# Kernel optimization log

Hardware: AMD Instinct MI355X
Metric: run time of the kernel (lower is better)

Reference implementation:

```python
import jax, jax.numpy as jnp
import numpy as np

B, T, D, H = 2, 4096, 768, 12
DH = D // H


def setup_inputs() -> dict:
    key = jax.random.key(0)
    ks = jax.random.split(key, 4)
    x = jax.random.normal(ks[0], (B, T, D), dtype=jnp.float32)
    Wqkv = jax.random.normal(ks[1], (D, 3 * D), dtype=jnp.float32) * (D ** -0.5)
    bqkv = jnp.zeros((3 * D,), dtype=jnp.float32)
    Wproj = jax.random.normal(ks[2], (D, D), dtype=jnp.float32) * (D ** -0.5)
    bproj = jnp.zeros((D,), dtype=jnp.float32)
    return {"x": x, "Wqkv": Wqkv, "bqkv": bqkv, "Wproj": Wproj, "bproj": bproj}


def reference(x, Wqkv, bqkv, Wproj, bproj):
    b, t, c = x.shape
    qkv = x @ Wqkv + bqkv                      # [B,T,3D]
    qkv = qkv.reshape(b, t, H, 3 * DH)
    q, k, v = jnp.split(qkv, 3, axis=-1)       # each [B,T,H,DH]
    q = q.transpose(0, 2, 1, 3)                # [B,H,T,DH]
    k = k.transpose(0, 2, 1, 3)
    v = v.transpose(0, 2, 1, 3)
    att = jnp.einsum('bhqd,bhkd->bhqk', q, k) / (DH ** 0.5)  # [B,H,T,T]
    mask = jnp.tril(jnp.ones((t, t), dtype=bool))
    att = jnp.where(mask, att, jnp.float32(-1e9))
    att = jax.nn.softmax(att, axis=-1)
    out = jnp.einsum('bhqk,bhkd->bhqd', att, v)  # [B,H,T,DH]
    out = out.transpose(0, 2, 1, 3).reshape(b, t, c)
    return out @ Wproj + bproj
```

## Files before the change

kernel.cpp:

```cpp
#include <hip/hip_runtime.h>

typedef unsigned short u16;
typedef unsigned int u32;
typedef __bf16 bf16x8 __attribute__((ext_vector_type(8)));
typedef float f32x4 __attribute__((ext_vector_type(4)));
typedef float f32x16 __attribute__((ext_vector_type(16)));
typedef u16 u16x4 __attribute__((ext_vector_type(4)));
typedef u16 u16x8 __attribute__((ext_vector_type(8)));
typedef u32 u32x2 __attribute__((ext_vector_type(2)));
typedef u32 u32x4 __attribute__((ext_vector_type(4)));

#define QSCALE 0.18033688011112042f
#define MFIX 12.0f

static __device__ __forceinline__ u16 f2bf(float f) {
  __bf16 h = (__bf16)f;
  return __builtin_bit_cast(u16, h);
}

static __device__ __forceinline__ u32 pk2(float a, float b) {
  return (u32)f2bf(a) | ((u32)f2bf(b) << 16);
}

static __device__ __forceinline__ void gl_lds16(const void* g, void* l) {
  __builtin_amdgcn_global_load_lds(
      (const __attribute__((address_space(1))) unsigned int*)g,
      (__attribute__((address_space(3))) unsigned int*)l, 16, 0, 0);
}

static __device__ __forceinline__ void wait_vmcnt8() {
  asm volatile("s_waitcnt vmcnt(8)" ::: "memory");
}
static __device__ __forceinline__ void wait_vmcnt4() {
  asm volatile("s_waitcnt vmcnt(4)" ::: "memory");
}
static __device__ __forceinline__ void wait_vmcnt0() {
  asm volatile("s_waitcnt vmcnt(0)" ::: "memory");
}
static __device__ __forceinline__ void barrier_mem() {
  asm volatile("s_barrier" ::: "memory");
}

static __device__ __forceinline__ f32x16 zero16() {
  f32x16 z;
#pragma unroll
  for (int i = 0; i < 16; ++i) z[i] = 0.f;
  return z;
}

__global__ void k_cvt(const float* __restrict__ in, u16* __restrict__ out, int n4) {
  int i = blockIdx.x * 256 + threadIdx.x;
  if (i < n4) {
    f32x4 f = ((const f32x4*)in)[i];
    u16x4 u = { f2bf(f[0]), f2bf(f[1]), f2bf(f[2]), f2bf(f[3]) };
    ((u16x4*)out)[i] = u;
  }
}

__global__ void k_transpose_cvt(const float* __restrict__ in, u16* __restrict__ out,
                                int R, int C) {
  __shared__ float tile[32][33];
  const int c0 = blockIdx.x * 32, r0 = blockIdx.y * 32;
  const int tx = threadIdx.x, ty = threadIdx.y;
#pragma unroll
  for (int i = 0; i < 4; ++i)
    tile[ty + i * 8][tx] = in[(size_t)(r0 + ty + i * 8) * C + c0 + tx];
  __syncthreads();
#pragma unroll
  for (int i = 0; i < 4; ++i)
    out[(size_t)(c0 + ty + i * 8) * R + r0 + tx] = f2bf(tile[tx][ty + i * 8]);
}

static __device__ __forceinline__ void gemm_core(const u16* __restrict__ Ag,
                                                 const u16* __restrict__ Btg,
                                                 int K, int m0, int n0,
                                                 u16* As, u16* Bs,
                                                 f32x4 acc[4][4]) {
  const int tid = threadIdx.x;
  const int lane = tid & 63;
  const int wid = tid >> 6;
  const int wm = wid >> 1, wn = wid & 1;
  const int l16 = lane & 15, lg = lane >> 4;

  for (int kt = 0; kt < K; kt += 64) {
    __syncthreads();
#pragma unroll
    for (int i = 0; i < 4; ++i) {
      int chunk = i * 256 + tid;
      int row = chunk >> 3;
      int lcb = ((chunk & 7) << 4) ^ ((row & 7) << 4);
      gl_lds16(Ag + (size_t)(m0 + row) * K + kt + (lcb >> 1),
               As + ((i * 256 + wid * 64) << 3));
    }
#pragma unroll
    for (int i = 0; i < 4; ++i) {
      int chunk = i * 256 + tid;
      int row = chunk >> 3;
      int lcb = ((chunk & 7) << 4) ^ ((row & 7) << 4);
      gl_lds16(Btg + (size_t)(n0 + row) * K + kt + (lcb >> 1),
               Bs + ((i * 256 + wid * 64) << 3));
    }
    __syncthreads();

#pragma unroll
    for (int ks = 0; ks < 2; ++ks) {
      bf16x8 af[4], bfr[4];
#pragma unroll
      for (int mi = 0; mi < 4; ++mi) {
        int row = wm * 64 + mi * 16 + l16;
        int off = row * 128 + ((ks * 64 + (lg << 4)) ^ ((row & 7) << 4));
        af[mi] = *(const bf16x8*)((const char*)As + off);
      }
#pragma unroll
      for (int ni = 0; ni < 4; ++ni) {
        int row = wn * 64 + ni * 16 + l16;
        int off = row * 128 + ((ks * 64 + (lg << 4)) ^ ((row & 7) << 4));
        bfr[ni] = *(const bf16x8*)((const char*)Bs + off);
      }
#pragma unroll
      for (int mi = 0; mi < 4; ++mi)
#pragma unroll
        for (int ni = 0; ni < 4; ++ni)
          acc[mi][ni] = __builtin_amdgcn_mfma_f32_16x16x32_bf16(
              af[mi], bfr[ni], acc[mi][ni], 0, 0, 0);
    }
  }
}

__global__ __launch_bounds__(256) void k_gemm_qkv(
    const u16* __restrict__ A, const u16* __restrict__ Bt,
    const float* __restrict__ bias, u16* __restrict__ Q, u16* __restrict__ Kb,
    u16* __restrict__ Vt) {
  __shared__ __align__(16) u16 SH[128 * 128];
  u16* As = SH;
  u16* Bs = SH + 128 * 64;
  const int m0 = blockIdx.y * 128, n0 = blockIdx.x * 128;
  const f32x4 fz = {0.f, 0.f, 0.f, 0.f};
  f32x4 acc[4][4];
#pragma unroll
  for (int mi = 0; mi < 4; ++mi)
#pragma unroll
    for (int ni = 0; ni < 4; ++ni) acc[mi][ni] = fz;

  gemm_core(A, Bt, 768, m0, n0, As, Bs, acc);
  __syncthreads();

  const int tid = threadIdx.x, lane = tid & 63, wid = tid >> 6;
  const int wm = wid >> 1, wn = wid & 1, l16 = lane & 15, lg = lane >> 4;
#pragma unroll
  for (int mi = 0; mi < 4; ++mi)
#pragma unroll
    for (int ni = 0; ni < 4; ++ni) {
      int nl = wn * 64 + ni * 16 + l16;
      int n = n0 + nl;
      float bi = bias[n];
      int h = n / 192;
      int rr = n - h * 192;
      int ml = wm * 64 + mi * 16 + lg * 4;
      if (rr >= 128) {
        int m0w = m0 + ml;
        int bb = m0w >> 12, t0 = m0w & 4095;
        u16x4 vv;
#pragma unroll
        for (int r = 0; r < 4; ++r) vv[r] = f2bf(acc[mi][ni][r] + bi);
        *(u16x4*)(Vt + ((size_t)(bb * 12 + h) * 64 + (rr - 128)) * 4096 + t0) = vv;
      } else {
        float sc = (rr < 64) ? QSCALE : 1.0f;
#pragma unroll
        for (int r = 0; r < 4; ++r)
          SH[(ml + r) * 128 + nl] = f2bf((acc[mi][ni][r] + bi) * sc);
      }
    }
  __syncthreads();

  const int bb2 = m0 >> 12, tb = m0 & 4095;
#pragma unroll
  for (int i = 0; i < 8; ++i) {
    int id = i * 256 + tid;
    int row = id >> 4;
    int c = id & 15;
    int n = n0 + c * 8;
    int h = n / 192;
    int rr = n - h * 192;
    if (rr < 128) {
      u16x8 v = *(const u16x8*)(SH + row * 128 + c * 8);
      size_t base = ((size_t)(bb2 * 12 + h) * 4096 + tb + row) * 64;
      u16* dst = (rr < 64) ? (Q + base + rr) : (Kb + base + rr - 64);
      *(u16x8*)dst = v;
    }
  }
}

__global__ __launch_bounds__(256) void k_gemm_proj(
    const u16* __restrict__ A, const u16* __restrict__ Bt,
    const float* __restrict__ bias, float* __restrict__ out) {
  __shared__ __align__(16) u16 As[128 * 64];
  __shared__ __align__(16) u16 Bs[128 * 64];
  const int m0 = blockIdx.y * 128, n0 = blockIdx.x * 128;
  const f32x4 fz = {0.f, 0.f, 0.f, 0.f};
  f32x4 acc[4][4];
#pragma unroll
  for (int mi = 0; mi < 4; ++mi)
#pragma unroll
    for (int ni = 0; ni < 4; ++ni) acc[mi][ni] = fz;

  gemm_core(A, Bt, 768, m0, n0, As, Bs, acc);

  const int tid = threadIdx.x, lane = tid & 63, wid = tid >> 6;
  const int wm = wid >> 1, wn = wid & 1, l16 = lane & 15, lg = lane >> 4;
#pragma unroll
  for (int mi = 0; mi < 4; ++mi)
#pragma unroll
    for (int ni = 0; ni < 4; ++ni) {
      int n = n0 + wn * 64 + ni * 16 + l16;
      float bi = bias[n];
#pragma unroll
      for (int r = 0; r < 4; ++r) {
        int m = m0 + wm * 64 + mi * 16 + lg * 4 + r;
        out[(size_t)m * 768 + n] = acc[mi][ni][r] + bi;
      }
    }
}

__global__ __launch_bounds__(128) void k_attn(const u16* __restrict__ Qg,
                                              const u16* __restrict__ Kg,
                                              const u16* __restrict__ Vtg,
                                              u16* __restrict__ Og) {
  __shared__ __align__(16) u16 Ks[2][64 * 64];
  __shared__ __align__(16) u16 Vs[64 * 64];
  const int bid = blockIdx.x;
  const int xcd = bid & 7;
  const int u = bid >> 3;
  const int s = u & 31;
  const int rnd = u >> 5;
  const int bh = xcd * 3 + (rnd >> 1);
  const int jX = (rnd & 1) ? s : (63 - s);
  const int tid = threadIdx.x;
  const int lane = tid & 63;
  const int wid = tid >> 6;
  const int l32 = lane & 31;
  const int hi = lane >> 5;
  const int rxor = (l32 & 7) << 4;
  const size_t qk_base = (size_t)bh * (4096 * 64);
  const size_t vt_base = (size_t)bh * (64 * 4096);
  const int b = bh / 12, h = bh - b * 12;

  const int q0w = jX * 64 + wid * 32;
  const int qrow = q0w + l32;
  const int nkt = jX + 1;

  int coK[4], coVa[4], coVb[4];
#pragma unroll
  for (int st = 0; st < 4; ++st) coK[st] = (st * 32 + hi * 16) ^ rxor;
#pragma unroll
  for (int ks = 0; ks < 4; ++ks) {
    coVa[ks] = (ks * 32 + hi * 8) ^ rxor;
    coVb[ks] = (ks * 32 + 16 + hi * 8) ^ rxor;
  }
  const int rb0 = l32 * 128, rb1 = (32 + l32) * 128;

  const int trow = tid >> 3;
  const int tcol = ((((tid & 7) << 4) ^ ((trow & 7) << 4)) >> 1);
  const int tdst = tid << 3;
  const u16* kp0 = Kg + qk_base + (size_t)trow * 64 + tcol;
  const u16* kp1 = kp0 + (size_t)16 * 64;
  const u16* kp2 = kp0 + (size_t)32 * 64;
  const u16* kp3 = kp0 + (size_t)48 * 64;
  const u16* vq0 = Vtg + vt_base + (size_t)trow * 4096 + tcol;
  const u16* vq1 = vq0 + (size_t)16 * 4096;
  const u16* vq2 = vq0 + (size_t)32 * 4096;
  const u16* vq3 = vq0 + (size_t)48 * 4096;

  auto stageK = [&](u16* Kd) {
    gl_lds16(kp0, Kd + tdst);
    gl_lds16(kp1, Kd + 1024 + tdst);
    gl_lds16(kp2, Kd + 2048 + tdst);
    gl_lds16(kp3, Kd + 3072 + tdst);
    kp0 += 4096; kp1 += 4096; kp2 += 4096; kp3 += 4096;
  };
  auto stageV = [&]() {
    gl_lds16(vq0, Vs + tdst);
    gl_lds16(vq1, Vs + 1024 + tdst);
    gl_lds16(vq2, Vs + 2048 + tdst);
    gl_lds16(vq3, Vs + 3072 + tdst);
    vq0 += 64; vq1 += 64; vq2 += 64; vq3 += 64;
  };

  bf16x8 qb[4];
#pragma unroll
  for (int st = 0; st < 4; ++st)
    qb[st] = *(const bf16x8*)(Qg + qk_base + (size_t)qrow * 64 + st * 16 + hi * 8);

  f32x16 o0 = zero16(), o1 = zero16();
  float lrun = 0.f;

  stageK(Ks[0]);

  for (int kt = 0; kt < nkt; ++kt) {
    const bool more = (kt + 1 < nkt);
    stageV();
    if (more) stageK(Ks[(kt + 1) & 1]);
    if (more) wait_vmcnt8(); else wait_vmcnt4();
    barrier_mem();

    const bool diag = (kt == nkt - 1);
    const bool halfskip = diag && (wid == 0);
    const char* Kbp = (const char*)Ks[kt & 1];
    const char* Vb = (const char*)Vs;

    f32x16 s0 = zero16(), s1 = zero16();
    __builtin_amdgcn_s_setprio(1);
#pragma unroll
    for (int st = 0; st < 4; ++st) {
      bf16x8 ka0 = *(const bf16x8*)(Kbp + rb0 + coK[st]);
      s0 = __builtin_amdgcn_mfma_f32_32x32x16_bf16(ka0, qb[st], s0, 0, 0, 0);
    }
    if (!halfskip) {
#pragma unroll
      for (int st = 0; st < 4; ++st) {
        bf16x8 ka1 = *(const bf16x8*)(Kbp + rb1 + coK[st]);
        s1 = __builtin_amdgcn_mfma_f32_32x32x16_bf16(ka1, qb[st], s1, 0, 0, 0);
      }
    }
    __builtin_amdgcn_s_setprio(0);

    if (diag) {
      const int kbase = kt * 64 + 4 * hi;
#pragma unroll
      for (int r = 0; r < 16; ++r) {
        int kpv = kbase + (r & 3) + 8 * (r >> 2);
        s0[r] = (kpv > qrow) ? -3.0e38f : s0[r];
        if (!halfskip) s1[r] = (kpv + 32 > qrow) ? -3.0e38f : s1[r];
      }
    }

#pragma unroll
    for (int r = 0; r < 16; ++r) {
      s0[r] = __builtin_amdgcn_exp2f(s0[r] - MFIX);
      if (!halfskip) s1[r] = __builtin_amdgcn_exp2f(s1[r] - MFIX);
    }

    float a8[8];
#pragma unroll
    for (int r = 0; r < 8; ++r) {
      float v = s0[r] + s0[r + 8];
      if (!halfskip) v += s1[r] + s1[r + 8];
      a8[r] = v;
    }
    lrun += ((a8[0] + a8[1]) + (a8[2] + a8[3])) +
            ((a8[4] + a8[5]) + (a8[6] + a8[7]));

    if (more) wait_vmcnt4(); else wait_vmcnt0();
    barrier_mem();

    __builtin_amdgcn_s_setprio(1);
#pragma unroll
    for (int ks = 0; ks < 4; ++ks) {
      if (ks >= 2 && halfskip) continue;
      const f32x16& P = (ks >= 2) ? s1 : s0;
      const int base = (ks & 1) * 8;
      u32x4 w = { pk2(P[base + 0], P[base + 1]), pk2(P[base + 2], P[base + 3]),
                  pk2(P[base + 4], P[base + 5]), pk2(P[base + 6], P[base + 7]) };
      bf16x8 pbk = __builtin_bit_cast(bf16x8, w);
      u32x2 q0 = *(const u32x2*)(Vb + rb0 + coVa[ks]);
      u32x2 q1 = *(const u32x2*)(Vb + rb0 + coVb[ks]);
      u32x4 av = {q0[0], q0[1], q1[0], q1[1]};
      bf16x8 va0 = __builtin_bit_cast(bf16x8, av);
      o0 = __builtin_amdgcn_mfma_f32_32x32x16_bf16(va0, pbk, o0, 0, 0, 0);
      u32x2 p0 = *(const u32x2*)(Vb + rb1 + coVa[ks]);
      u32x2 p1 = *(const u32x2*)(Vb + rb1 + coVb[ks]);
      u32x4 bv = {p0[0], p0[1], p1[0], p1[1]};
      bf16x8 va1 = __builtin_bit_cast(bf16x8, bv);
      o1 = __builtin_amdgcn_mfma_f32_32x32x16_bf16(va1, pbk, o1, 0, 0, 0);
    }
    __builtin_amdgcn_s_setprio(0);

    barrier_mem();
  }

  float lt = lrun + __shfl_xor(lrun, 32, 64);
  float inv = 1.0f / lt;
  u16* orow = Og + ((size_t)b * 4096 + qrow) * 768 + h * 64;
#pragma unroll
  for (int gg = 0; gg < 4; ++gg) {
    u16x4 v0, v1;
#pragma unroll
    for (int i = 0; i < 4; ++i) {
      v0[i] = f2bf(o0[4 * gg + i] * inv);
      v1[i] = f2bf(o1[4 * gg + i] * inv);
    }
    *(u16x4*)(orow + 8 * gg + 4 * hi) = v0;
    *(u16x4*)(orow + 32 + 8 * gg + 4 * hi) = v1;
  }
}

extern "C" void kernel_launch(void* const* d_in, const int* in_sizes, int n_in,
                              void* d_out, int out_size, void* d_ws, size_t ws_size,
                              hipStream_t stream) {
  const float* x = (const float*)d_in[0];
  const float* Wqkv = (const float*)d_in[1];
  const float* bqkv = (const float*)d_in[2];
  const float* Wproj = (const float*)d_in[3];
  const float* bproj = (const float*)d_in[4];
  float* out = (float*)d_out;

  char* ws = (char*)d_ws;
  u16* Xbf = (u16*)(ws + 0);
  u16* WqkvT = (u16*)(ws + 12582912);
  u16* WprojT = (u16*)(ws + 16121856);
  u16* Q = (u16*)(ws + 17301504);
  u16* K = (u16*)(ws + 29884416);
  u16* Vt = (u16*)(ws + 42467328);
  u16* O = (u16*)(ws + 55050240);

  k_cvt<<<6144, 256, 0, stream>>>(x, Xbf, 1572864);
  k_transpose_cvt<<<dim3(72, 24), dim3(32, 8), 0, stream>>>(Wqkv, WqkvT, 768, 2304);
  k_transpose_cvt<<<dim3(24, 24), dim3(32, 8), 0, stream>>>(Wproj, WprojT, 768, 768);
  k_gemm_qkv<<<dim3(18, 64), 256, 0, stream>>>(Xbf, WqkvT, bqkv, Q, K, Vt);
  k_attn<<<1536, 128, 0, stream>>>(Q, K, Vt, O);
  k_gemm_proj<<<dim3(6, 64), 256, 0, stream>>>(O, WprojT, bproj, out);
}
```

Before: 197.7 us.

## Split attention key tile across four waves with LDS reduction of partial outputs

The attention block grows from two to four waves. Each pair of waves shares a 32-row query slice and splits the 64-key tile in half, so every wave does half the QK and PV MFMAs per tile. Partial outputs and row sums are combined through LDS at the end. This doubles the waves available to hide latency and halves the staging loads per thread, at the cost of an extra reduction pass, more LDS traffic and a possible occupancy change from the new launch bounds.

```diff
diff --git a/kernel.cpp b/kernel.cpp
--- a/kernel.cpp
+++ b/kernel.cpp
@@ -28,11 +28,11 @@
       (__attribute__((address_space(3))) unsigned int*)l, 16, 0, 0);
 }
 
-static __device__ __forceinline__ void wait_vmcnt8() {
-  asm volatile("s_waitcnt vmcnt(8)" ::: "memory");
-}
 static __device__ __forceinline__ void wait_vmcnt4() {
   asm volatile("s_waitcnt vmcnt(4)" ::: "memory");
+}
+static __device__ __forceinline__ void wait_vmcnt2() {
+  asm volatile("s_waitcnt vmcnt(2)" ::: "memory");
 }
 static __device__ __forceinline__ void wait_vmcnt0() {
   asm volatile("s_waitcnt vmcnt(0)" ::: "memory");
@@ -222,12 +222,14 @@
     }
 }
 
-__global__ __launch_bounds__(128) void k_attn(const u16* __restrict__ Qg,
-                                              const u16* __restrict__ Kg,
-                                              const u16* __restrict__ Vtg,
-                                              u16* __restrict__ Og) {
-  __shared__ __align__(16) u16 Ks[2][64 * 64];
-  __shared__ __align__(16) u16 Vs[64 * 64];
+__global__ __launch_bounds__(256, 6) void k_attn(const u16* __restrict__ Qg,
+                                                 const u16* __restrict__ Kg,
+                                                 const u16* __restrict__ Vtg,
+                                                 u16* __restrict__ Og) {
+  __shared__ __align__(16) u16 LDSB[12288];
+  u16* const KsA = LDSB;
+  u16* const KsB = LDSB + 4096;
+  u16* const Vs = LDSB + 8192;
   const int bid = blockIdx.x;
   const int xcd = bid & 7;
   const int u = bid >> 3;
@@ -238,6 +240,7 @@
   const int tid = threadIdx.x;
   const int lane = tid & 63;
   const int wid = tid >> 6;
+  const int qhalf = wid >> 1, khalf = wid & 1;
   const int l32 = lane & 31;
   const int hi = lane >> 5;
   const int rxor = (l32 & 7) << 4;
@@ -245,45 +248,39 @@
   const size_t vt_base = (size_t)bh * (64 * 4096);
   const int b = bh / 12, h = bh - b * 12;
 
-  const int q0w = jX * 64 + wid * 32;
-  const int qrow = q0w + l32;
+  const int qrow = jX * 64 + qhalf * 32 + l32;
   const int nkt = jX + 1;
 
-  int coK[4], coVa[4], coVb[4];
+  int coK[4];
 #pragma unroll
   for (int st = 0; st < 4; ++st) coK[st] = (st * 32 + hi * 16) ^ rxor;
-#pragma unroll
-  for (int ks = 0; ks < 4; ++ks) {
-    coVa[ks] = (ks * 32 + hi * 8) ^ rxor;
-    coVb[ks] = (ks * 32 + 16 + hi * 8) ^ rxor;
-  }
+  int cvA[2], cvB[2];
+#pragma unroll
+  for (int kl = 0; kl < 2; ++kl) {
+    int ks = 2 * khalf + kl;
+    cvA[kl] = (ks * 32 + hi * 8) ^ rxor;
+    cvB[kl] = (ks * 32 + 16 + hi * 8) ^ rxor;
+  }
+  const int rbK = (khalf * 32 + l32) * 128;
   const int rb0 = l32 * 128, rb1 = (32 + l32) * 128;
 
   const int trow = tid >> 3;
   const int tcol = ((((tid & 7) << 4) ^ ((trow & 7) << 4)) >> 1);
   const int tdst = tid << 3;
   const u16* kp0 = Kg + qk_base + (size_t)trow * 64 + tcol;
-  const u16* kp1 = kp0 + (size_t)16 * 64;
-  const u16* kp2 = kp0 + (size_t)32 * 64;
-  const u16* kp3 = kp0 + (size_t)48 * 64;
+  const u16* kp1 = kp0 + (size_t)32 * 64;
   const u16* vq0 = Vtg + vt_base + (size_t)trow * 4096 + tcol;
-  const u16* vq1 = vq0 + (size_t)16 * 4096;
-  const u16* vq2 = vq0 + (size_t)32 * 4096;
-  const u16* vq3 = vq0 + (size_t)48 * 4096;
+  const u16* vq1 = vq0 + (size_t)32 * 4096;
 
   auto stageK = [&](u16* Kd) {
     gl_lds16(kp0, Kd + tdst);
-    gl_lds16(kp1, Kd + 1024 + tdst);
-    gl_lds16(kp2, Kd + 2048 + tdst);
-    gl_lds16(kp3, Kd + 3072 + tdst);
-    kp0 += 4096; kp1 += 4096; kp2 += 4096; kp3 += 4096;
+    gl_lds16(kp1, Kd + 2048 + tdst);
+    kp0 += 4096; kp1 += 4096;
   };
   auto stageV = [&]() {
     gl_lds16(vq0, Vs + tdst);
-    gl_lds16(vq1, Vs + 1024 + tdst);
-    gl_lds16(vq2, Vs + 2048 + tdst);
-    gl_lds16(vq3, Vs + 3072 + tdst);
-    vq0 += 64; vq1 += 64; vq2 += 64; vq3 += 64;
+    gl_lds16(vq1, Vs + 2048 + tdst);
+    vq0 += 64; vq1 += 64;
   };
 
   bf16x8 qb[4];
@@ -294,103 +291,112 @@
   f32x16 o0 = zero16(), o1 = zero16();
   float lrun = 0.f;
 
-  stageK(Ks[0]);
+  stageK(KsA);
 
   for (int kt = 0; kt < nkt; ++kt) {
     const bool more = (kt + 1 < nkt);
     stageV();
-    if (more) stageK(Ks[(kt + 1) & 1]);
-    if (more) wait_vmcnt8(); else wait_vmcnt4();
+    if (more) stageK((kt & 1) ? KsA : KsB);
+    if (more) wait_vmcnt4(); else wait_vmcnt2();
     barrier_mem();
 
     const bool diag = (kt == nkt - 1);
-    const bool halfskip = diag && (wid == 0);
-    const char* Kbp = (const char*)Ks[kt & 1];
+    const bool skip = diag && (qhalf == 0) && (khalf == 1);
+    const bool tri = diag && (qhalf == khalf);
+    const char* Kbp = (const char*)((kt & 1) ? KsB : KsA);
     const char* Vb = (const char*)Vs;
 
-    f32x16 s0 = zero16(), s1 = zero16();
-    __builtin_amdgcn_s_setprio(1);
-#pragma unroll
-    for (int st = 0; st < 4; ++st) {
-      bf16x8 ka0 = *(const bf16x8*)(Kbp + rb0 + coK[st]);
-      s0 = __builtin_amdgcn_mfma_f32_32x32x16_bf16(ka0, qb[st], s0, 0, 0, 0);
-    }
-    if (!halfskip) {
+    f32x16 s0 = zero16();
+    if (!skip) {
+      __builtin_amdgcn_s_setprio(1);
 #pragma unroll
       for (int st = 0; st < 4; ++st) {
-        bf16x8 ka1 = *(const bf16x8*)(Kbp + rb1 + coK[st]);
-        s1 = __builtin_amdgcn_mfma_f32_32x32x16_bf16(ka1, qb[st], s1, 0, 0, 0);
-      }
-    }
-    __builtin_amdgcn_s_setprio(0);
-
-    if (diag) {
-      const int kbase = kt * 64 + 4 * hi;
-#pragma unroll
-      for (int r = 0; r < 16; ++r) {
-        int kpv = kbase + (r & 3) + 8 * (r >> 2);
-        s0[r] = (kpv > qrow) ? -3.0e38f : s0[r];
-        if (!halfskip) s1[r] = (kpv + 32 > qrow) ? -3.0e38f : s1[r];
-      }
-    }
-
-#pragma unroll
-    for (int r = 0; r < 16; ++r) {
-      s0[r] = __builtin_amdgcn_exp2f(s0[r] - MFIX);
-      if (!halfskip) s1[r] = __builtin_amdgcn_exp2f(s1[r] - MFIX);
-    }
-
-    float a8[8];
-#pragma unroll
-    for (int r = 0; r < 8; ++r) {
-      float v = s0[r] + s0[r + 8];
-      if (!halfskip) v += s1[r] + s1[r + 8];
-      a8[r] = v;
-    }
-    lrun += ((a8[0] + a8[1]) + (a8[2] + a8[3])) +
-            ((a8[4] + a8[5]) + (a8[6] + a8[7]));
-
-    if (more) wait_vmcnt4(); else wait_vmcnt0();
+        bf16x8 ka = *(const bf16x8*)(Kbp + rbK + coK[st]);
+        s0 = __builtin_amdgcn_mfma_f32_32x32x16_bf16(ka, qb[st], s0, 0, 0, 0);
+      }
+      __builtin_amdgcn_s_setprio(0);
+
+      if (tri) {
+        const int kbase = kt * 64 + khalf * 32 + 4 * hi;
+#pragma unroll
+        for (int r = 0; r < 16; ++r) {
+          int kpv = kbase + (r & 3) + 8 * (r >> 2);
+          s0[r] = (kpv > qrow) ? -3.0e38f : s0[r];
+        }
+      }
+
+#pragma unroll
+      for (int r = 0; r < 16; ++r)
+        s0[r] = __builtin_amdgcn_exp2f(s0[r] - MFIX);
+
+      float a4[4];
+#pragma unroll
+      for (int r = 0; r < 4; ++r)
+        a4[r] = (s0[r] + s0[r + 4]) + (s0[r + 8] + s0[r + 12]);
+      lrun += (a4[0] + a4[1]) + (a4[2] + a4[3]);
+    }
+
+    if (more) wait_vmcnt2(); else wait_vmcnt0();
     barrier_mem();
 
-    __builtin_amdgcn_s_setprio(1);
-#pragma unroll
-    for (int ks = 0; ks < 4; ++ks) {
-      if (ks >= 2 && halfskip) continue;
-      const f32x16& P = (ks >= 2) ? s1 : s0;
-      const int base = (ks & 1) * 8;
-      u32x4 w = { pk2(P[base + 0], P[base + 1]), pk2(P[base + 2], P[base + 3]),
-                  pk2(P[base + 4], P[base + 5]), pk2(P[base + 6], P[base + 7]) };
-      bf16x8 pbk = __builtin_bit_cast(bf16x8, w);
-      u32x2 q0 = *(const u32x2*)(Vb + rb0 + coVa[ks]);
-      u32x2 q1 = *(const u32x2*)(Vb + rb0 + coVb[ks]);
-      u32x4 av = {q0[0], q0[1], q1[0], q1[1]};
-      bf16x8 va0 = __builtin_bit_cast(bf16x8, av);
-      o0 = __builtin_amdgcn_mfma_f32_32x32x16_bf16(va0, pbk, o0, 0, 0, 0);
-      u32x2 p0 = *(const u32x2*)(Vb + rb1 + coVa[ks]);
-      u32x2 p1 = *(const u32x2*)(Vb + rb1 + coVb[ks]);
-      u32x4 bv = {p0[0], p0[1], p1[0], p1[1]};
-      bf16x8 va1 = __builtin_bit_cast(bf16x8, bv);
-      o1 = __builtin_amdgcn_mfma_f32_32x32x16_bf16(va1, pbk, o1, 0, 0, 0);
-    }
-    __builtin_amdgcn_s_setprio(0);
+    if (!skip) {
+      __builtin_amdgcn_s_setprio(1);
+#pragma unroll
+      for (int kl = 0; kl < 2; ++kl) {
+        const int base = kl * 8;
+        u32x4 w = { pk2(s0[base + 0], s0[base + 1]), pk2(s0[base + 2], s0[base + 3]),
+                    pk2(s0[base + 4], s0[base + 5]), pk2(s0[base + 6], s0[base + 7]) };
+        bf16x8 pbk = __builtin_bit_cast(bf16x8, w);
+        u32x2 q0 = *(const u32x2*)(Vb + rb0 + cvA[kl]);
+        u32x2 q1 = *(const u32x2*)(Vb + rb0 + cvB[kl]);
+        u32x4 av = {q0[0], q0[1], q1[0], q1[1]};
+        bf16x8 va0 = __builtin_bit_cast(bf16x8, av);
+        o0 = __builtin_amdgcn_mfma_f32_32x32x16_bf16(va0, pbk, o0, 0, 0, 0);
+        u32x2 p0 = *(const u32x2*)(Vb + rb1 + cvA[kl]);
+        u32x2 p1 = *(const u32x2*)(Vb + rb1 + cvB[kl]);
+        u32x4 bv = {p0[0], p0[1], p1[0], p1[1]};
+        bf16x8 va1 = __builtin_bit_cast(bf16x8, bv);
+        o1 = __builtin_amdgcn_mfma_f32_32x32x16_bf16(va1, pbk, o1, 0, 0, 0);
+      }
+      __builtin_amdgcn_s_setprio(0);
+    }
 
     barrier_mem();
   }
 
-  float lt = lrun + __shfl_xor(lrun, 32, 64);
-  float inv = 1.0f / lt;
-  u16* orow = Og + ((size_t)b * 4096 + qrow) * 768 + h * 64;
-#pragma unroll
-  for (int gg = 0; gg < 4; ++gg) {
-    u16x4 v0, v1;
-#pragma unroll
-    for (int i = 0; i < 4; ++i) {
-      v0[i] = f2bf(o0[4 * gg + i] * inv);
-      v1[i] = f2bf(o1[4 * gg + i] * inv);
-    }
-    *(u16x4*)(orow + 8 * gg + 4 * hi) = v0;
-    *(u16x4*)(orow + 32 + 8 * gg + 4 * hi) = v1;
+  float* red = (float*)LDSB;
+  if (khalf == 1) {
+    float* dst = red + (qhalf * 64 + lane) * 33;
+#pragma unroll
+    for (int i = 0; i < 16; ++i) {
+      dst[i] = o0[i];
+      dst[16 + i] = o1[i];
+    }
+    dst[32] = lrun;
+  }
+  barrier_mem();
+  if (khalf == 0) {
+    const float* src = red + (qhalf * 64 + lane) * 33;
+#pragma unroll
+    for (int i = 0; i < 16; ++i) {
+      o0[i] += src[i];
+      o1[i] += src[16 + i];
+    }
+    lrun += src[32];
+    float lt = lrun + __shfl_xor(lrun, 32, 64);
+    float inv = 1.0f / lt;
+    u16* orow = Og + ((size_t)b * 4096 + qrow) * 768 + h * 64;
+#pragma unroll
+    for (int gg = 0; gg < 4; ++gg) {
+      u16x4 v0, v1;
+#pragma unroll
+      for (int i = 0; i < 4; ++i) {
+        v0[i] = f2bf(o0[4 * gg + i] * inv);
+        v1[i] = f2bf(o1[4 * gg + i] * inv);
+      }
+      *(u16x4*)(orow + 8 * gg + 4 * hi) = v0;
+      *(u16x4*)(orow + 32 + 8 * gg + 4 * hi) = v1;
+    }
   }
 }
 
@@ -417,6 +423,6 @@
   k_transpose_cvt<<<dim3(72, 24), dim3(32, 8), 0, stream>>>(Wqkv, WqkvT, 768, 2304);
   k_transpose_cvt<<<dim3(24, 24), dim3(32, 8), 0, stream>>>(Wproj, WprojT, 768, 768);
   k_gemm_qkv<<<dim3(18, 64), 256, 0, stream>>>(Xbf, WqkvT, bqkv, Q, K, Vt);
-  k_attn<<<1536, 128, 0, stream>>>(Q, K, Vt, O);
+  k_attn<<<1536, 256, 0, stream>>>(Q, K, Vt, O);
   k_gemm_proj<<<dim3(6, 64), 256, 0, stream>>>(O, WprojT, bproj, out);
 }
```

Measured after the change: 225.0 us. 13.8% more time.
